# Kernel optimization log

Measured on AMD Instinct MI355X. Metric: run time of the kernel, lower is better.

The kernel has to match this reference:

```python
import jax, jax.numpy as jnp
import numpy as np

B, C, W, H = 4, 256, 64, 64
K = C // 8      # key_channels = in_channels // 8
O = C           # out_channels = in_channels


def setup_inputs() -> dict:
    key = jax.random.key(0)
    ks = jax.random.split(key, 8)
    x = jax.random.normal(ks[0], (B, C, W, H), dtype=jnp.float32)
    # 1x1 conv weights stored as [out, in]; conv-style fan-in init scale
    s = 1.0 / np.sqrt(C)
    Wq = jax.random.uniform(ks[1], (K, C), minval=-s, maxval=s, dtype=jnp.float32)
    bq = jax.random.uniform(ks[2], (K,), minval=-s, maxval=s, dtype=jnp.float32)
    Wk = jax.random.uniform(ks[3], (K, C), minval=-s, maxval=s, dtype=jnp.float32)
    bk = jax.random.uniform(ks[4], (K,), minval=-s, maxval=s, dtype=jnp.float32)
    Wv = jax.random.uniform(ks[5], (O, C), minval=-s, maxval=s, dtype=jnp.float32)
    bv = jax.random.uniform(ks[6], (O,), minval=-s, maxval=s, dtype=jnp.float32)
    # gamma is zero-init in the module; use a small nonzero value so the
    # attention branch contributes measurably (kernel-testing baseline)
    gamma = 0.1 * jax.random.normal(ks[7], (1,), dtype=jnp.float32)
    return {"x": x, "Wq": Wq, "bq": bq, "Wk": Wk, "bk": bk,
            "Wv": Wv, "bv": bv, "gamma": gamma}


def reference(x, Wq, bq, Wk, bk, Wv, bv, gamma):
    b, c, w, h = x.shape
    n = w * h
    xr = x.reshape(b, c, n)                                   # B,C,N
    # 1x1 convs == per-pixel linear projections
    q = jnp.einsum('kc,bcn->bnk', Wq, xr) + bq                # B,N,K (permuted query)
    k = jnp.einsum('kc,bcn->bkn', Wk, xr) + bk[:, None]       # B,K,N
    energy = jnp.einsum('bnk,bkm->bnm', q, k)                 # B,N,N
    attention = jax.nn.softmax(energy, axis=-1)
    v = jnp.einsum('oc,bcn->bon', Wv, xr) + bv[:, None]       # B,O,N
    # out = bmm(V, attention^T): out[b,o,m] = sum_n V[b,o,n] * attn[b,m,n]
    out = jnp.einsum('bon,bmn->bom', v, attention)
    out = out.reshape(b, O, w, h)
    out = gamma * out + x                                     # true skip connection
    return out, attention
```

## Files before the change

### kernel.cpp

```cpp
#include <hip/hip_runtime.h>

#define NB  4
#define CCH 256
#define NN  4096
#define KD  32
#define OD  256

typedef __attribute__((ext_vector_type(8))) __bf16 bf16x8;
typedef __attribute__((ext_vector_type(4))) float  floatx4;

__device__ __forceinline__ unsigned short f2bf(float f) {
    union { float f; unsigned u; } v; v.f = f;
    unsigned r = v.u + 0x7FFFu + ((v.u >> 16) & 1u);
    return (unsigned short)(r >> 16);
}

__global__ __launch_bounds__(256) void proj_kernel(
    const float* __restrict__ x,
    const float* __restrict__ Wq, const float* __restrict__ bq,
    const float* __restrict__ Wk, const float* __restrict__ bk,
    const float* __restrict__ Wv, const float* __restrict__ bv,
    unsigned short* __restrict__ Qb, unsigned short* __restrict__ Ktb,
    unsigned short* __restrict__ Vb)
{
    __shared__ __align__(16) float WL[32 * CCH];

    const int chunk = blockIdx.x;
    const int ntile = blockIdx.y;
    const int b     = blockIdx.z;
    const int tid   = threadIdx.x;
    const int n     = ntile * 256 + tid;

    const float* Wsrc;
    const float* bsrc;
    if (chunk == 0)      { Wsrc = Wq; bsrc = bq; }
    else if (chunk == 1) { Wsrc = Wk; bsrc = bk; }
    else                 { Wsrc = Wv + (size_t)(chunk - 2) * 32 * CCH;
                           bsrc = bv + (chunk - 2) * 32; }

    #pragma unroll
    for (int i = 0; i < 8; ++i) {
        int idx4 = i * 256 + tid;
        *(floatx4*)(WL + idx4 * 4) = *(const floatx4*)(Wsrc + idx4 * 4);
    }
    __syncthreads();

    float acc[32];
    #pragma unroll
    for (int j = 0; j < 32; ++j) acc[j] = bsrc[j];

    const float* xp = x + (size_t)b * CCH * NN + n;
    for (int c = 0; c < CCH; c += 4) {
        float xv0 = xp[(size_t)(c + 0) * NN];
        float xv1 = xp[(size_t)(c + 1) * NN];
        float xv2 = xp[(size_t)(c + 2) * NN];
        float xv3 = xp[(size_t)(c + 3) * NN];
        #pragma unroll
        for (int j = 0; j < 32; ++j) {
            floatx4 w = *(const floatx4*)(WL + j * CCH + c);
            acc[j] += w[0] * xv0;
            acc[j] += w[1] * xv1;
            acc[j] += w[2] * xv2;
            acc[j] += w[3] * xv3;
        }
    }

    if (chunk < 2) {
        unsigned short* dst = (chunk ? Ktb : Qb) + (size_t)(b * NN + n) * KD;
        __align__(16) unsigned short tmp[32];
        #pragma unroll
        for (int j = 0; j < 32; ++j) tmp[j] = f2bf(acc[j]);
        #pragma unroll
        for (int i = 0; i < 4; ++i)
            ((bf16x8*)dst)[i] = ((const bf16x8*)tmp)[i];
    } else {
        const int o0 = (chunk - 2) * 32;
        #pragma unroll
        for (int j = 0; j < 32; ++j)
            Vb[(size_t)(b * OD + o0 + j) * NN + n] = f2bf(acc[j]);
    }
}

__global__ __launch_bounds__(256, 2) void attn_kernel(
    const float* __restrict__ x, const float* __restrict__ gammap,
    const unsigned short* __restrict__ Qb,
    const unsigned short* __restrict__ Ktb,
    const unsigned short* __restrict__ Vb,
    float* __restrict__ out, float* __restrict__ attn)
{
    __shared__ __align__(16) unsigned char smem[63744];
    unsigned short* Vlds  = (unsigned short*)smem;
    float*          panel = (float*)(smem + 40960);
    unsigned short* Pl    = (unsigned short*)(smem + 58368);
    float*          sred  = (float*)(smem + 63488);

    const int tid  = threadIdx.x;
    const int wave = tid >> 6;
    const int lane = tid & 63;
    const int quad = lane >> 4;
    const int li   = lane & 15;
    const int g    = wave & 1;
    const int h    = wave >> 1;

    const int b  = blockIdx.x >> 7;
    const int mw = (blockIdx.x & 127) * 32;
    const int hb = h * 2048;

    unsigned short* Vh   = Vlds + h * 10240;
    float*          pan  = panel + wave * 1088;
    unsigned short* Plds = Pl + wave * 640;

    const floatx4 zero = {0.f, 0.f, 0.f, 0.f};

    const bf16x8 aQ = *(const bf16x8*)(Qb + (size_t)(b * NN + mw + g * 16 + li) * KD + quad * 8);
    const unsigned short* ktbase = Ktb + (size_t)b * NN * KD + quad * 8;

    float lrow[4] = {0.f, 0.f, 0.f, 0.f};
    #pragma unroll 4
    for (int nt = 0; nt < 128; ++nt) {
        bf16x8 bK = *(const bf16x8*)(ktbase + (size_t)(hb + nt * 16 + li) * KD);
        floatx4 s = __builtin_amdgcn_mfma_f32_16x16x32_bf16(aQ, bK, zero, 0, 0, 0);
        #pragma unroll
        for (int r = 0; r < 4; ++r) lrow[r] += __expf(s[r]);
    }
    #pragma unroll
    for (int r = 0; r < 4; ++r) {
        #pragma unroll
        for (int xm = 1; xm < 16; xm <<= 1)
            lrow[r] += __shfl_xor(lrow[r], xm);
    }
    if (li == 0) {
        #pragma unroll
        for (int r = 0; r < 4; ++r) sred[(g * 2 + h) * 16 + quad * 4 + r] = lrow[r];
    }
    __syncthreads();
    float linv[4];
    #pragma unroll
    for (int r = 0; r < 4; ++r) {
        const int row = quad * 4 + r;
        linv[r] = 1.0f / (sred[(g * 2 + 0) * 16 + row] + sred[(g * 2 + 1) * 16 + row]);
    }

    floatx4 oacc[16];
    #pragma unroll
    for (int ot = 0; ot < 16; ++ot) oacc[ot] = zero;

    const int hs = tid >> 7;
    const int st = tid & 127;
    const unsigned short* vsrc = Vb + (size_t)b * OD * NN + hs * 2048;
    unsigned short*       vdst = Vlds + hs * 10240;

    for (int c = 0; c < 64; ++c) {
        const int n0 = hb + c * 32;
        bf16x8 bK0 = *(const bf16x8*)(ktbase + (size_t)(n0 + li) * KD);
        bf16x8 bK1 = *(const bf16x8*)(ktbase + (size_t)(n0 + 16 + li) * KD);

        __syncthreads();
        bf16x8 vtmp[8];
        #pragma unroll
        for (int i = 0; i < 8; ++i) {
            int linear = i * 128 + st;
            int o = linear >> 2, p = linear & 3;
            vtmp[i] = *(const bf16x8*)(vsrc + (size_t)o * NN + c * 32 + p * 8);
        }
        #pragma unroll
        for (int i = 0; i < 8; ++i) {
            int linear = i * 128 + st;
            int o = linear >> 2, p = linear & 3;
            *(bf16x8*)(vdst + o * 40 + p * 8) = vtmp[i];
        }
        __syncthreads();

        floatx4 s0 = __builtin_amdgcn_mfma_f32_16x16x32_bf16(aQ, bK0, zero, 0, 0, 0);
        floatx4 s1 = __builtin_amdgcn_mfma_f32_16x16x32_bf16(aQ, bK1, zero, 0, 0, 0);
        const int cc = c & 1;
        #pragma unroll
        for (int r = 0; r < 4; ++r) {
            float p0 = __expf(s0[r]) * linv[r];
            float p1 = __expf(s1[r]) * linv[r];
            const int row = quad * 4 + r;
            pan[row * 68 + cc * 32 + li]      = p0;
            pan[row * 68 + cc * 32 + 16 + li] = p1;
            Plds[row * 40 + li]      = f2bf(p0);
            Plds[row * 40 + 16 + li] = f2bf(p1);
        }
        bf16x8 aP = *(const bf16x8*)(Plds + li * 40 + quad * 8);
        #pragma unroll
        for (int ot = 0; ot < 16; ++ot) {
            bf16x8 bV = *(const bf16x8*)(Vh + (ot * 16 + li) * 40 + quad * 8);
            oacc[ot] = __builtin_amdgcn_mfma_f32_16x16x32_bf16(aP, bV, oacc[ot], 0, 0, 0);
        }
        if (cc) {
            float* ab = attn + ((size_t)(b * NN + mw + g * 16)) * NN + hb + (c - 1) * 32;
            #pragma unroll
            for (int it = 0; it < 4; ++it) {
                int row = it * 4 + quad;
                floatx4 v = *(const floatx4*)(pan + row * 68 + li * 4);
                *(floatx4*)(ab + (size_t)row * NN + li * 4) = v;
            }
        }
    }

    __syncthreads();
    float* Olds = (float*)(void*)smem;
    if (h == 0) {
        #pragma unroll
        for (int ot = 0; ot < 16; ++ot)
            #pragma unroll
            for (int r = 0; r < 4; ++r)
                Olds[(ot * 16 + li) * 36 + g * 16 + quad * 4 + r] = oacc[ot][r];
    }
    __syncthreads();
    if (h == 1) {
        #pragma unroll
        for (int ot = 0; ot < 16; ++ot)
            #pragma unroll
            for (int r = 0; r < 4; ++r)
                Olds[(ot * 16 + li) * 36 + g * 16 + quad * 4 + r] += oacc[ot][r];
    }
    __syncthreads();
    const float gm = gammap[0];
    #pragma unroll
    for (int it = 0; it < 8; ++it) {
        int linear = it * 256 + tid;
        int o = linear >> 3, seg = linear & 7;
        floatx4 ov = *(const floatx4*)(Olds + o * 36 + seg * 4);
        size_t gidx = (size_t)(b * OD + o) * NN + mw + seg * 4;
        floatx4 xv = *(const floatx4*)(x + gidx);
        floatx4 res;
        res[0] = gm * ov[0] + xv[0];
        res[1] = gm * ov[1] + xv[1];
        res[2] = gm * ov[2] + xv[2];
        res[3] = gm * ov[3] + xv[3];
        *(floatx4*)(out + gidx) = res;
    }
}

extern "C" void kernel_launch(void* const* d_in, const int* in_sizes, int n_in,
                              void* d_out, int out_size, void* d_ws, size_t ws_size,
                              hipStream_t stream) {
    const float* x     = (const float*)d_in[0];
    const float* Wq    = (const float*)d_in[1];
    const float* bq    = (const float*)d_in[2];
    const float* Wk    = (const float*)d_in[3];
    const float* bk    = (const float*)d_in[4];
    const float* Wv    = (const float*)d_in[5];
    const float* bv    = (const float*)d_in[6];
    const float* gamma = (const float*)d_in[7];

    float* out  = (float*)d_out;
    float* attn = out + (size_t)NB * OD * NN;

    unsigned short* Qb  = (unsigned short*)d_ws;
    unsigned short* Ktb = Qb  + (size_t)NB * NN * KD;
    unsigned short* Vb  = Ktb + (size_t)NB * NN * KD;

    proj_kernel<<<dim3(10, 16, 4), 256, 0, stream>>>(x, Wq, bq, Wk, bk, Wv, bv, Qb, Ktb, Vb);
    attn_kernel<<<dim3(512), 256, 0, stream>>>(x, gamma, Qb, Ktb, Vb, out, attn);
}
```

Measured before the change: 462.4 us.

## Rewrite projection kernel with split-bf16 MFMA GEMM tiles

Result: faster. 440.0 us (-4.8%).

```diff
diff --git a/kernel.cpp b/kernel.cpp
--- a/kernel.cpp
+++ b/kernel.cpp
@@ -14,6 +14,21 @@
     unsigned r = v.u + 0x7FFFu + ((v.u >> 16) & 1u);
     return (unsigned short)(r >> 16);
 }
+__device__ __forceinline__ float bf2f(unsigned short h) {
+    union { unsigned u; float f; } v; v.u = ((unsigned)h) << 16;
+    return v.f;
+}
+__device__ __forceinline__ bf16x8 ldfrag(const unsigned short* p) {
+    union { bf16x8 v; unsigned u[4]; } r;
+    r.u[0] = *(const unsigned*)(p + 0);
+    r.u[1] = *(const unsigned*)(p + 2);
+    r.u[2] = *(const unsigned*)(p + 4);
+    r.u[3] = *(const unsigned*)(p + 6);
+    return r.v;
+}
+
+#define WPAD 66
+#define VPAD 136
 
 __global__ __launch_bounds__(256) void proj_kernel(
     const float* __restrict__ x,
@@ -23,61 +38,155 @@
     unsigned short* __restrict__ Qb, unsigned short* __restrict__ Ktb,
     unsigned short* __restrict__ Vb)
 {
-    __shared__ __align__(16) float WL[32 * CCH];
-
-    const int chunk = blockIdx.x;
-    const int ntile = blockIdx.y;
-    const int b     = blockIdx.z;
-    const int tid   = threadIdx.x;
-    const int n     = ntile * 256 + tid;
-
-    const float* Wsrc;
-    const float* bsrc;
-    if (chunk == 0)      { Wsrc = Wq; bsrc = bq; }
-    else if (chunk == 1) { Wsrc = Wk; bsrc = bk; }
-    else                 { Wsrc = Wv + (size_t)(chunk - 2) * 32 * CCH;
-                           bsrc = bv + (chunk - 2) * 32; }
-
-    #pragma unroll
-    for (int i = 0; i < 8; ++i) {
-        int idx4 = i * 256 + tid;
-        *(floatx4*)(WL + idx4 * 4) = *(const floatx4*)(Wsrc + idx4 * 4);
-    }
-    __syncthreads();
-
-    float acc[32];
-    #pragma unroll
-    for (int j = 0; j < 32; ++j) acc[j] = bsrc[j];
-
-    const float* xp = x + (size_t)b * CCH * NN + n;
-    for (int c = 0; c < CCH; c += 4) {
-        float xv0 = xp[(size_t)(c + 0) * NN];
-        float xv1 = xp[(size_t)(c + 1) * NN];
-        float xv2 = xp[(size_t)(c + 2) * NN];
-        float xv3 = xp[(size_t)(c + 3) * NN];
-        #pragma unroll
-        for (int j = 0; j < 32; ++j) {
-            floatx4 w = *(const floatx4*)(WL + j * CCH + c);
-            acc[j] += w[0] * xv0;
-            acc[j] += w[1] * xv1;
-            acc[j] += w[2] * xv2;
-            acc[j] += w[3] * xv3;
-        }
-    }
-
-    if (chunk < 2) {
-        unsigned short* dst = (chunk ? Ktb : Qb) + (size_t)(b * NN + n) * KD;
-        __align__(16) unsigned short tmp[32];
-        #pragma unroll
-        for (int j = 0; j < 32; ++j) tmp[j] = f2bf(acc[j]);
-        #pragma unroll
-        for (int i = 0; i < 4; ++i)
-            ((bf16x8*)dst)[i] = ((const bf16x8*)tmp)[i];
+    __shared__ __align__(16) unsigned char smem[50944];
+    unsigned short* Wh   = (unsigned short*)smem;
+    unsigned short* Wl   = (unsigned short*)(smem + 8448);
+    unsigned short* Xth  = (unsigned short*)(smem + 16896);
+    unsigned short* Xtl  = (unsigned short*)(smem + 33792);
+    float*          bias = (float*)(smem + 50688);
+    unsigned short* Yt = (unsigned short*)(smem + 16896);
+    unsigned short* Vt = (unsigned short*)(smem + 16896);
+
+    const int mc  = blockIdx.x;
+    const int nb  = blockIdx.y;
+    const int b   = blockIdx.z;
+    const int tid = threadIdx.x;
+    const int wave = tid >> 6;
+    const int lane = tid & 63;
+    const int quad = lane >> 4;
+    const int li   = lane & 15;
+    const int pxw  = wave * 32;
+    const int px0  = nb * 128;
+
+    const float* xb = x + (size_t)b * CCH * NN;
+
+    floatx4 acc[4][2];
+    #pragma unroll
+    for (int mf = 0; mf < 4; ++mf)
+        #pragma unroll
+        for (int nf = 0; nf < 2; ++nf)
+            acc[mf][nf] = (floatx4){0.f, 0.f, 0.f, 0.f};
+
+    for (int ks = 0; ks < 4; ++ks) {
+        const int c0 = ks * 64;
+        __syncthreads();
+
+        #pragma unroll
+        for (int i = 0; i < 4; ++i) {
+            int idx4 = i * 256 + tid;
+            int row  = idx4 >> 4;
+            int c4   = (idx4 & 15) * 4;
+            const float* src;
+            if (mc == 0) src = (row < 32) ? (Wq + row * CCH) : (Wk + (row - 32) * CCH);
+            else         src = Wv + ((size_t)((mc - 1) * 64 + row)) * CCH;
+            floatx4 w = *(const floatx4*)(src + c0 + c4);
+            #pragma unroll
+            for (int j = 0; j < 4; ++j) {
+                unsigned short h = f2bf(w[j]);
+                unsigned short l = f2bf(w[j] - bf2f(h));
+                Wh[row * WPAD + c4 + j] = h;
+                Wl[row * WPAD + c4 + j] = l;
+            }
+        }
+        #pragma unroll
+        for (int i = 0; i < 8; ++i) {
+            int idx4 = i * 256 + tid;
+            int c    = idx4 >> 5;
+            int px   = (idx4 & 31) * 4;
+            floatx4 v = *(const floatx4*)(xb + (size_t)(c0 + c) * NN + px0 + px);
+            #pragma unroll
+            for (int j = 0; j < 4; ++j) {
+                unsigned short h = f2bf(v[j]);
+                unsigned short l = f2bf(v[j] - bf2f(h));
+                Xth[(px + j) * WPAD + c] = h;
+                Xtl[(px + j) * WPAD + c] = l;
+            }
+        }
+        if (ks == 0 && tid < 64) {
+            float bb;
+            if (mc == 0) bb = (tid < 32) ? bq[tid] : bk[tid - 32];
+            else         bb = bv[(mc - 1) * 64 + tid];
+            bias[tid] = bb;
+        }
+        __syncthreads();
+
+        #pragma unroll
+        for (int kk = 0; kk < 2; ++kk) {
+            bf16x8 ah[4], al[4], bh[2], bl[2];
+            #pragma unroll
+            for (int mf = 0; mf < 4; ++mf) {
+                const int ro = (mf * 16 + li) * WPAD + kk * 32 + quad * 8;
+                ah[mf] = ldfrag(Wh + ro);
+                al[mf] = ldfrag(Wl + ro);
+            }
+            #pragma unroll
+            for (int nf = 0; nf < 2; ++nf) {
+                const int ro = (pxw + nf * 16 + li) * WPAD + kk * 32 + quad * 8;
+                bh[nf] = ldfrag(Xth + ro);
+                bl[nf] = ldfrag(Xtl + ro);
+            }
+            #pragma unroll
+            for (int mf = 0; mf < 4; ++mf)
+                #pragma unroll
+                for (int nf = 0; nf < 2; ++nf) {
+                    acc[mf][nf] = __builtin_amdgcn_mfma_f32_16x16x32_bf16(ah[mf], bh[nf], acc[mf][nf], 0, 0, 0);
+                    acc[mf][nf] = __builtin_amdgcn_mfma_f32_16x16x32_bf16(ah[mf], bl[nf], acc[mf][nf], 0, 0, 0);
+                    acc[mf][nf] = __builtin_amdgcn_mfma_f32_16x16x32_bf16(al[mf], bh[nf], acc[mf][nf], 0, 0, 0);
+                }
+        }
+    }
+
+    __syncthreads();
+    if (mc == 0) {
+        #pragma unroll
+        for (int mf = 0; mf < 4; ++mf)
+            #pragma unroll
+            for (int nf = 0; nf < 2; ++nf)
+                #pragma unroll
+                for (int r = 0; r < 4; ++r) {
+                    const int o = mf * 16 + quad * 4 + r;
+                    float f = acc[mf][nf][r] + bias[o];
+                    Yt[(pxw + nf * 16 + li) * WPAD + o] = f2bf(f);
+                }
+        __syncthreads();
+        if (tid < 128) {
+            const int px = tid;
+            const size_t n = (size_t)(b * NN + px0 + px);
+            unsigned short* qdst = Qb  + n * KD;
+            unsigned short* kdst = Ktb + n * KD;
+            const unsigned short* src = Yt + px * WPAD;
+            #pragma unroll
+            for (int i = 0; i < 4; ++i) {
+                union { uint4 u4; unsigned u[4]; } q, k;
+                #pragma unroll
+                for (int j = 0; j < 4; ++j) {
+                    q.u[j] = *(const unsigned*)(src + i * 8 + j * 2);
+                    k.u[j] = *(const unsigned*)(src + 32 + i * 8 + j * 2);
+                }
+                *(uint4*)(qdst + i * 8) = q.u4;
+                *(uint4*)(kdst + i * 8) = k.u4;
+            }
+        }
     } else {
-        const int o0 = (chunk - 2) * 32;
-        #pragma unroll
-        for (int j = 0; j < 32; ++j)
-            Vb[(size_t)(b * OD + o0 + j) * NN + n] = f2bf(acc[j]);
+        #pragma unroll
+        for (int mf = 0; mf < 4; ++mf)
+            #pragma unroll
+            for (int nf = 0; nf < 2; ++nf)
+                #pragma unroll
+                for (int r = 0; r < 4; ++r) {
+                    const int o = mf * 16 + quad * 4 + r;
+                    float f = acc[mf][nf][r] + bias[o];
+                    Vt[o * VPAD + pxw + nf * 16 + li] = f2bf(f);
+                }
+        __syncthreads();
+        const int ol   = tid >> 2;
+        const int part = tid & 3;
+        const unsigned short* src = Vt + ol * VPAD + part * 32;
+        unsigned short* dst = Vb + (size_t)(b * OD + (mc - 1) * 64 + ol) * NN + px0 + part * 32;
+        *(uint4*)(dst + 0) = *(const uint4*)(src + 0);
+        *(uint4*)(dst + 8) = *(const uint4*)(src + 8);
+        *(uint4*)(dst + 16) = *(const uint4*)(src + 16);
+        *(uint4*)(dst + 24) = *(const uint4*)(src + 24);
     }
 }
 
@@ -255,6 +364,6 @@
     unsigned short* Ktb = Qb  + (size_t)NB * NN * KD;
     unsigned short* Vb  = Ktb + (size_t)NB * NN * KD;
 
-    proj_kernel<<<dim3(10, 16, 4), 256, 0, stream>>>(x, Wq, bq, Wk, bk, Wv, bv, Qb, Ktb, Vb);
+    proj_kernel<<<dim3(5, 32, 4), 256, 0, stream>>>(x, Wq, bq, Wk, bk, Wv, bv, Qb, Ktb, Vb);
     attn_kernel<<<dim3(512), 256, 0, stream>>>(x, gamma, Qb, Ktb, Vb, out, attn);
 }
```
